# Performance work log

Hardware: AMD Instinct MI355X
Metric: run time of the kernel (lower is better)

Reference implementation:

```python
import jax, jax.numpy as jnp
import numpy as np

B, S, D, H = 8, 1024, 1024, 16
DK = D // H  # 64


def setup_inputs() -> dict:
    key = jax.random.key(0)
    ks = jax.random.split(key, 12)
    def w(k):
        return (jax.random.normal(k, (D, D), dtype=jnp.float32) * 0.02)
    def b(k):
        return (jax.random.normal(k, (D,), dtype=jnp.float32) * 0.02)
    return {
        "q": jax.random.normal(ks[0], (B, S, D), dtype=jnp.float32),
        "k": jax.random.normal(ks[1], (B, S, D), dtype=jnp.float32),
        "v": jax.random.normal(ks[2], (B, S, D), dtype=jnp.float32),
        "mask": jax.random.randint(ks[3], (B, 1, S, S), 0, 2, dtype=jnp.int32),
        "WQ_w": w(ks[4]), "WQ_b": b(ks[5]),
        "WK_w": w(ks[6]), "WK_b": b(ks[7]),
        "WV_w": w(ks[8]), "WV_b": b(ks[9]),
        "WO_w": w(ks[10]), "WO_b": b(ks[11]),
    }


def reference(q, k, v, mask, WQ_w, WQ_b, WK_w, WK_b, WV_w, WV_b, WO_w, WO_b):
    # nn.Linear: y = x @ W.T + b
    Q = (q @ WQ_w.T + WQ_b).reshape(B, S, H, DK)
    K = (k @ WK_w.T + WK_b).reshape(B, S, H, DK)
    V = (v @ WV_w.T + WV_b).reshape(B, S, H, DK)
    # scores: [B, H, Sq, Sk]
    scores = jnp.einsum("bqhd,bkhd->bhqk", Q, K) / jnp.sqrt(jnp.float32(DK))
    scores = jnp.where(mask == 0, jnp.float32(-1e9), scores)
    attn = jax.nn.softmax(scores, axis=-1)
    # dropout p=0.0 -> identity
    out = jnp.einsum("bhqk,bkhd->bqhd", attn, V).reshape(B, S, D)
    return out @ WO_w.T + WO_b
```

## Files before the change

### kernel.cpp

```cpp
#include <hip/hip_runtime.h>
#include <math.h>

typedef __bf16 bf16;
typedef __bf16 bf16x8 __attribute__((ext_vector_type(8)));
typedef __bf16 bf16x4 __attribute__((ext_vector_type(4)));
typedef float f32x4 __attribute__((ext_vector_type(4)));
typedef float f32x16 __attribute__((ext_vector_type(16)));
typedef int i32x4 __attribute__((ext_vector_type(4)));

constexpr int B_ = 8, S_ = 1024, D_ = 1024, H_ = 16, DK_ = 64;
constexpr int M_ = B_ * S_;
constexpr size_t A8 = (size_t)1 << 23;
constexpr size_t W1 = (size_t)1 << 20;
constexpr float QSCALE = 0.18033688011112042f;

#if __has_builtin(__builtin_amdgcn_exp2f)
#define EXP2F(x) __builtin_amdgcn_exp2f(x)
#else
#define EXP2F(x) exp2f(x)
#endif
#if __has_builtin(__builtin_amdgcn_rcpf)
#define RCPF(x) __builtin_amdgcn_rcpf(x)
#else
#define RCPF(x) (1.0f / (x))
#endif

#define GAS(p) ((const __attribute__((address_space(1))) void*)(p))
#define LAS(p) ((__attribute__((address_space(3))) void*)(p))

__device__ __forceinline__ float xor32f(float v, int bpidx) {
    return __builtin_bit_cast(float,
        __builtin_amdgcn_ds_bpermute(bpidx, __builtin_bit_cast(int, v)));
}
__device__ __forceinline__ int xor32i(int v, int bpidx) {
    return __builtin_amdgcn_ds_bpermute(bpidx, v);
}
__device__ __forceinline__ int pack_bf16(bf16 lo, bf16 hi) {
    return (int)(unsigned)__builtin_bit_cast(unsigned short, lo)
         | ((int)(unsigned)__builtin_bit_cast(unsigned short, hi) << 16);
}

struct F4Q { f32x4 a, b, c, d; };

__global__ __launch_bounds__(256) void cvt_all(
    const float* __restrict__ q, const float* __restrict__ k,
    const float* __restrict__ v, const float* __restrict__ w0,
    const float* __restrict__ w1, const float* __restrict__ w2,
    const float* __restrict__ w3, bf16* __restrict__ dst)
{
    size_t e = ((size_t)blockIdx.x * 256 + threadIdx.x) * 8;
    const float* src;
    size_t off;
    if (e < 3 * A8) {
        int t = (int)(e >> 23);
        src = (t == 0) ? q : (t == 1) ? k : v;
        off = e & (A8 - 1);
    } else {
        size_t ew = e - 3 * A8;
        int t = (int)(ew >> 20);
        src = (t == 0) ? w0 : (t == 1) ? w1 : (t == 2) ? w2 : w3;
        off = ew & (W1 - 1);
    }
    float4 a = *(const float4*)(src + off);
    float4 b = *(const float4*)(src + off + 4);
    bf16x8 o = { (bf16)a.x, (bf16)a.y, (bf16)a.z, (bf16)a.w,
                 (bf16)b.x, (bf16)b.y, (bf16)b.z, (bf16)b.w };
    *(bf16x8*)(dst + e) = o;
}

__global__ __launch_bounds__(256) void mask_cvt(
    const int* __restrict__ mask, float* __restrict__ mf)
{
    const int bx = blockIdx.x;
    const int kt = bx & 15, qt = (bx >> 4) & 7, b = bx >> 7;
    const int tid = threadIdx.x;
    const int w = tid >> 6, lane = tid & 63;
    const int hi = lane >> 5, l31 = lane & 31;
    const int q = qt * 128 + w * 32 + l31;

    const int* src = mask + ((size_t)b << 20) + (size_t)q * 1024 + kt * 64 + hi * 4;
    float* dst = mf + (size_t)bx * 8192 + w * 2048 + lane * 4;
#pragma unroll
    for (int blk = 0; blk < 2; ++blk)
#pragma unroll
        for (int rr = 0; rr < 4; ++rr) {
            int4 m = *(const int4*)(src + blk * 32 + rr * 8);
            f32x4 o = { m.x ? 0.f : -1e9f, m.y ? 0.f : -1e9f,
                        m.z ? 0.f : -1e9f, m.w ? 0.f : -1e9f };
            *(f32x4*)(dst + (blk * 4 + rr) * 256) = o;
        }
}

template<int OUT_MODE>
__global__ __launch_bounds__(256) void gemm_mfma(
    const bf16* __restrict__ X, const bf16* __restrict__ W,
    const float* __restrict__ bias, void* __restrict__ outv, float oscale)
{
    constexpr int K = 1024;
    __shared__ bf16 As[128 * 32];
    __shared__ bf16 Bs[128 * 32];

    const int tid  = threadIdx.x;
    const int lane = tid & 63;
    const int w    = tid >> 6;
    const int wm   = w & 1, wn = w >> 1;
    const int quad = lane >> 4, l15 = lane & 15;
    const int bm = blockIdx.x * 128, bn = blockIdx.y * 128;

    f32x4 acc[4][4];
#pragma unroll
    for (int i = 0; i < 4; ++i)
#pragma unroll
        for (int j = 0; j < 4; ++j)
#pragma unroll
            for (int r = 0; r < 4; ++r) acc[i][j][r] = 0.f;

    const int lrow = lane >> 2;
    const int lcol = (lane & 3) * 8;

    for (int k0 = 0; k0 < K; k0 += 32) {
        __syncthreads();
#pragma unroll
        for (int i = 0; i < 2; ++i) {
            const int rbase = w * 16 + i * 64;
            __builtin_amdgcn_global_load_lds(
                GAS(X + (size_t)(bm + rbase + lrow) * K + k0 + lcol),
                LAS(As + rbase * 32), 16, 0, 0);
            __builtin_amdgcn_global_load_lds(
                GAS(W + (size_t)(bn + rbase + lrow) * K + k0 + lcol),
                LAS(Bs + rbase * 32), 16, 0, 0);
        }
        __syncthreads();

        bf16x8 a[4], b[4];
#pragma unroll
        for (int i = 0; i < 4; ++i)
            a[i] = *(const bf16x8*)(As + (wm * 64 + i * 16 + l15) * 32 + quad * 8);
#pragma unroll
        for (int j = 0; j < 4; ++j)
            b[j] = *(const bf16x8*)(Bs + (wn * 64 + j * 16 + l15) * 32 + quad * 8);
#pragma unroll
        for (int i = 0; i < 4; ++i)
#pragma unroll
            for (int j = 0; j < 4; ++j)
                acc[i][j] = __builtin_amdgcn_mfma_f32_16x16x32_bf16(
                    a[i], b[j], acc[i][j], 0, 0, 0);
    }

#pragma unroll
    for (int i = 0; i < 4; ++i) {
#pragma unroll
        for (int j = 0; j < 4; ++j) {
            const int n = bn + wn * 64 + j * 16 + l15;
            const float bs = bias[n];
            if (OUT_MODE == 2) {
                const int m0 = bm + wm * 64 + i * 16 + quad * 4;
                const int bb = m0 >> 10, s0 = m0 & 1023;
                const int h = n >> 6, dk = n & 63;
                bf16x4 o;
#pragma unroll
                for (int r = 0; r < 4; ++r) o[r] = (bf16)(acc[i][j][r] + bs);
                *(bf16x4*)((bf16*)outv + (((size_t)(bb * 16 + h) * 64 + dk) << 10) + s0) = o;
            } else {
#pragma unroll
                for (int r = 0; r < 4; ++r) {
                    const int m = bm + wm * 64 + i * 16 + quad * 4 + r;
                    const float val = acc[i][j][r] + bs;
                    if (OUT_MODE == 0) {
                        ((float*)outv)[(size_t)m * 1024 + n] = val;
                    } else {
                        const int bb = m >> 10, s = m & 1023;
                        const int h = n >> 6, dk = n & 63;
                        ((bf16*)outv)[(((size_t)(bb * 16 + h)) * 1024 + s) * 64 + dk] =
                            (bf16)(val * oscale);
                    }
                }
            }
        }
    }
}

__global__ __launch_bounds__(256) void attn_mfma(
    const bf16* __restrict__ Q, const bf16* __restrict__ Kt,
    const bf16* __restrict__ Vt, const float* __restrict__ mf,
    bf16* __restrict__ out)
{
    __shared__ bf16 smem[2 * 2 * 4096];

    const int tid  = threadIdx.x;
    const int lane = tid & 63;
    const int w    = tid >> 6;
    const int hi   = lane >> 5, l31 = lane & 31;

    const int wid = (blockIdx.x & 7) * 128 + (blockIdx.x >> 3);
    const int qt = wid & 7;
    const int h  = (wid >> 3) & 15;
    const int b  = wid >> 7;

    const bf16* Qg  = Q + ((size_t)((b * H_ + h) * S_) + qt * 128 + w * 32) * DK_;
    const char* Kgh = (const char*)(Kt + (size_t)(b * H_ + h) * S_ * DK_);
    const char* Vgh = (const char*)(Vt + ((size_t)(b * H_ + h) << 16));
    const float* mtb = mf + (size_t)((b * 8 + qt) * 16) * 8192 + w * 2048 + lane * 4;

    const int tA = tid,        rA = tA >> 3, cA = (tA & 7) * 16;
    const int tB = 256 + tid,  rB = tB >> 3, cB = (tB & 7) * 16;
    const int kSrcA = rA * 128  + (cA ^ ((rA & 7) << 4));
    const int kSrcB = rB * 128  + (cB ^ ((rB & 7) << 4));
    const int vSrcA = rA * 2048 + (cA ^ ((rA & 7) << 4));
    const int vSrcB = rB * 2048 + (cB ^ ((rB & 7) << 4));

    auto stage = [&](int buf, int tkt) {
        bf16* Ks = smem + buf * 8192;
        bf16* Vs = Ks + 4096;
        const char* kg = Kgh + (size_t)tkt * 8192;
        const char* vg = Vgh + (size_t)tkt * 128;
        __builtin_amdgcn_global_load_lds(GAS(kg + kSrcA), LAS(Ks + w * 512),        16, 0, 0);
        __builtin_amdgcn_global_load_lds(GAS(kg + kSrcB), LAS(Ks + 2048 + w * 512), 16, 0, 0);
        __builtin_amdgcn_global_load_lds(GAS(vg + vSrcA), LAS(Vs + w * 512),        16, 0, 0);
        __builtin_amdgcn_global_load_lds(GAS(vg + vSrcB), LAS(Vs + 2048 + w * 512), 16, 0, 0);
    };

    stage(0, 0);

    bf16x8 qf[4];
#pragma unroll
    for (int ks = 0; ks < 4; ++ks)
        qf[ks] = *(const bf16x8*)(Qg + (size_t)l31 * 64 + ks * 16 + hi * 8);

    f32x4 mreg[8];
#pragma unroll
    for (int i = 0; i < 8; ++i) mreg[i] = *(const f32x4*)(mtb + i * 256);

    f32x16 O0, O1;
#pragma unroll
    for (int r = 0; r < 16; ++r) { O0[r] = 0.f; O1[r] = 0.f; }
    float mrow = -INFINITY, lrowv = 0.f;
    const int bpidx = (lane ^ 32) << 2;
    const int swz = (l31 & 7) << 4;

    __syncthreads();

#pragma unroll 2
    for (int kt = 0; kt < 16; ++kt) {
        const int buf = kt & 1;
        const bf16* Ks = smem + buf * 8192;
        const bf16* Vs = Ks + 4096;
        const char* KsB = (const char*)Ks;
        const char* VsB = (const char*)Vs;

        F4Q mq0 = { mreg[0], mreg[1], mreg[2], mreg[3] };
        F4Q mq1 = { mreg[4], mreg[5], mreg[6], mreg[7] };
        f32x16 acc0 = __builtin_bit_cast(f32x16, mq0);
        f32x16 acc1 = __builtin_bit_cast(f32x16, mq1);

        if (kt < 15) {
            const float* mkn = mtb + (size_t)(kt + 1) * 8192;
#pragma unroll
            for (int i = 0; i < 8; ++i) mreg[i] = *(const f32x4*)(mkn + i * 256);
        }

        if (kt + 1 < 16) stage(buf ^ 1, kt + 1);

#pragma unroll
        for (int ks = 0; ks < 4; ++ks) {
            const int cb = ks * 32 + hi * 16;
            bf16x8 k0 = *(const bf16x8*)(KsB + l31 * 128        + (cb ^ swz));
            bf16x8 k1 = *(const bf16x8*)(KsB + (l31 + 32) * 128 + (cb ^ swz));
            acc0 = __builtin_amdgcn_mfma_f32_32x32x16_bf16(k0, qf[ks], acc0, 0, 0, 0);
            acc1 = __builtin_amdgcn_mfma_f32_32x32x16_bf16(k1, qf[ks], acc1, 0, 0, 0);
        }

        float red[8];
#pragma unroll
        for (int i = 0; i < 8; ++i)
            red[i] = fmaxf(fmaxf(acc0[i], acc0[i + 8]), fmaxf(acc1[i], acc1[i + 8]));
#pragma unroll
        for (int i = 0; i < 4; ++i) red[i] = fmaxf(red[i], red[i + 4]);
        float mx = fmaxf(fmaxf(red[0], red[1]), fmaxf(red[2], red[3]));
        mx = fmaxf(mx, xor32f(mx, bpidx));

        if (__any(mx > mrow + 8.0f)) {
            const float mn = fmaxf(mrow, mx);
            const float alpha = EXP2F(mrow - mn);
            mrow = mn;
            lrowv *= alpha;
#pragma unroll
            for (int r = 0; r < 16; ++r) { O0[r] *= alpha; O1[r] *= alpha; }
        }

#pragma unroll
        for (int r = 0; r < 16; ++r) acc0[r] = EXP2F(acc0[r] - mrow);
#pragma unroll
        for (int r = 0; r < 16; ++r) acc1[r] = EXP2F(acc1[r] - mrow);

        int wd0[8], wd1[8];
        float ps = 0.f;
#pragma unroll
        for (int s = 0; s < 8; ++s) {
            bf16 e0 = (bf16)acc0[2 * s], o0 = (bf16)acc0[2 * s + 1];
            bf16 e1 = (bf16)acc1[2 * s], o1 = (bf16)acc1[2 * s + 1];
            ps += (float)e0 + (float)o0 + (float)e1 + (float)o1;
            wd0[s] = pack_bf16(e0, o0);
            wd1[s] = pack_bf16(e1, o1);
        }
        ps += xor32f(ps, bpidx);
        lrowv += ps;

#pragma unroll
        for (int ks = 0; ks < 4; ++ks) {
            const int s0 = (ks & 1) * 4;
            int p0, p1, p2, p3;
            if (ks < 2) { p0 = wd0[s0]; p1 = wd0[s0 + 1]; p2 = wd0[s0 + 2]; p3 = wd0[s0 + 3]; }
            else        { p0 = wd1[s0]; p1 = wd1[s0 + 1]; p2 = wd1[s0 + 2]; p3 = wd1[s0 + 3]; }
            const int rx = xor32i(hi ? p0 : p2, bpidx);
            const int ry = xor32i(hi ? p1 : p3, bpidx);
            i32x4 pw = { hi ? rx : p0, hi ? ry : p1, hi ? p2 : rx, hi ? p3 : ry };
            bf16x8 pa = __builtin_bit_cast(bf16x8, pw);

            const int cb = ks * 32 + hi * 16;
            bf16x8 v0 = *(const bf16x8*)(VsB + l31 * 128        + (cb ^ swz));
            bf16x8 v1 = *(const bf16x8*)(VsB + (l31 + 32) * 128 + (cb ^ swz));
            O0 = __builtin_amdgcn_mfma_f32_32x32x16_bf16(v0, pa, O0, 0, 0, 0);
            O1 = __builtin_amdgcn_mfma_f32_32x32x16_bf16(v1, pa, O1, 0, 0, 0);
        }
        __syncthreads();
    }

    const float rinv = RCPF(lrowv);
    bf16* og = out + ((size_t)b * S_ + qt * 128 + w * 32 + l31) * D_ + h * DK_;
#pragma unroll
    for (int rr = 0; rr < 4; ++rr) {
        bf16x4 o0 = { (bf16)(O0[rr * 4 + 0] * rinv), (bf16)(O0[rr * 4 + 1] * rinv),
                      (bf16)(O0[rr * 4 + 2] * rinv), (bf16)(O0[rr * 4 + 3] * rinv) };
        bf16x4 o1 = { (bf16)(O1[rr * 4 + 0] * rinv), (bf16)(O1[rr * 4 + 1] * rinv),
                      (bf16)(O1[rr * 4 + 2] * rinv), (bf16)(O1[rr * 4 + 3] * rinv) };
        *(bf16x4*)(og + rr * 8 + hi * 4)      = o0;
        *(bf16x4*)(og + 32 + rr * 8 + hi * 4) = o1;
    }
}

extern "C" void kernel_launch(void* const* d_in, const int* in_sizes, int n_in,
                              void* d_out, int out_size, void* d_ws, size_t ws_size,
                              hipStream_t stream) {
    const float* q    = (const float*)d_in[0];
    const float* k    = (const float*)d_in[1];
    const float* v    = (const float*)d_in[2];
    const int*   mask = (const int*)d_in[3];
    const float* WQw  = (const float*)d_in[4];
    const float* WQb  = (const float*)d_in[5];
    const float* WKw  = (const float*)d_in[6];
    const float* WKb  = (const float*)d_in[7];
    const float* WVw  = (const float*)d_in[8];
    const float* WVb  = (const float*)d_in[9];
    const float* WOw  = (const float*)d_in[10];
    const float* WOb  = (const float*)d_in[11];

    bf16* ws = (bf16*)d_ws;
    bf16* qb  = ws;
    bf16* kb  = qb + A8;
    bf16* vb  = kb + A8;
    bf16* wqb = vb + A8;
    bf16* wkb = wqb + W1;
    bf16* wvb = wkb + W1;
    bf16* wob = wvb + W1;
    bf16* Qp  = wob + W1;
    bf16* Kp  = Qp + A8;
    bf16* Vp  = Kp + A8;
    float* maskf = (float*)qb;
    bf16* AO     = vb;

    cvt_all<<<dim3(14336), 256, 0, stream>>>(q, k, v, WQw, WKw, WVw, WOw, ws);

    dim3 gg(M_ / 128, D_ / 128);
    gemm_mfma<1><<<gg, 256, 0, stream>>>(qb, wqb, WQb, (void*)Qp, QSCALE);
    gemm_mfma<1><<<gg, 256, 0, stream>>>(kb, wkb, WKb, (void*)Kp, 1.0f);
    gemm_mfma<2><<<gg, 256, 0, stream>>>(vb, wvb, WVb, (void*)Vp, 1.0f);

    mask_cvt<<<dim3(1024), 256, 0, stream>>>(mask, maskf);

    attn_mfma<<<dim3(1024), 256, 0, stream>>>(Qp, Kp, Vp, maskf, AO);

    gemm_mfma<0><<<gg, 256, 0, stream>>>(AO, wob, WOb, d_out, 1.0f);
}
```

Measured before the change: 363.7 us.

## Merge QKV projections into one launch and tune attention inner loop

Folds the three separate Q/K/V projection GEMM launches into a single 1536-block launch that picks its operands by block index, and gives the output projection its own non-templated kernel. The attention kernel gets launch_bounds occupancy 4, s_setprio raised around the MFMA sections, a vectorised elementwise-max reduction, and a row sum taken from the packed bf16 words instead of converting each value back to float. These target launch overhead and tail effects in the projections and VALU cost in the softmax. The occupancy hint may force register spills, and the setprio and reduction changes could just as easily slow things down.

```diff
diff --git a/kernel.cpp b/kernel.cpp
--- a/kernel.cpp
+++ b/kernel.cpp
@@ -4,8 +4,11 @@
 typedef __bf16 bf16;
 typedef __bf16 bf16x8 __attribute__((ext_vector_type(8)));
 typedef __bf16 bf16x4 __attribute__((ext_vector_type(4)));
+typedef float f32x2 __attribute__((ext_vector_type(2)));
 typedef float f32x4 __attribute__((ext_vector_type(4)));
+typedef float f32x8 __attribute__((ext_vector_type(8)));
 typedef float f32x16 __attribute__((ext_vector_type(16)));
+typedef int i32x2 __attribute__((ext_vector_type(2)));
 typedef int i32x4 __attribute__((ext_vector_type(4)));
 
 constexpr int B_ = 8, S_ = 1024, D_ = 1024, H_ = 16, DK_ = 64;
@@ -91,21 +94,33 @@
         }
 }
 
-template<int OUT_MODE>
-__global__ __launch_bounds__(256) void gemm_mfma(
-    const bf16* __restrict__ X, const bf16* __restrict__ W,
-    const float* __restrict__ bias, void* __restrict__ outv, float oscale)
+__global__ __launch_bounds__(256) void qkv_gemm(
+    const bf16* __restrict__ qb, const bf16* __restrict__ kb,
+    const bf16* __restrict__ vb, const bf16* __restrict__ wq,
+    const bf16* __restrict__ wk, const bf16* __restrict__ wv,
+    const float* __restrict__ bq, const float* __restrict__ bk,
+    const float* __restrict__ bv, bf16* __restrict__ Qp,
+    bf16* __restrict__ Kp, bf16* __restrict__ Vp, float qscale)
 {
     constexpr int K = 1024;
     __shared__ bf16 As[128 * 32];
     __shared__ bf16 Bs[128 * 32];
+
+    const int bid = blockIdx.x;
+    const int which = bid >> 9;
+    const int gb = bid & 511;
+    const bf16* X = which == 0 ? qb : which == 1 ? kb : vb;
+    const bf16* W = which == 0 ? wq : which == 1 ? wk : wv;
+    const float* bias = which == 0 ? bq : which == 1 ? bk : bv;
+    bf16* outp = which == 0 ? Qp : which == 1 ? Kp : Vp;
+    const float oscale = which == 0 ? qscale : 1.0f;
 
     const int tid  = threadIdx.x;
     const int lane = tid & 63;
     const int w    = tid >> 6;
     const int wm   = w & 1, wn = w >> 1;
     const int quad = lane >> 4, l15 = lane & 15;
-    const int bm = blockIdx.x * 128, bn = blockIdx.y * 128;
+    const int bm = (gb & 63) * 128, bn = (gb >> 6) * 128;
 
     f32x4 acc[4][4];
 #pragma unroll
@@ -153,34 +168,98 @@
         for (int j = 0; j < 4; ++j) {
             const int n = bn + wn * 64 + j * 16 + l15;
             const float bs = bias[n];
-            if (OUT_MODE == 2) {
+            if (which == 2) {
                 const int m0 = bm + wm * 64 + i * 16 + quad * 4;
                 const int bb = m0 >> 10, s0 = m0 & 1023;
                 const int h = n >> 6, dk = n & 63;
                 bf16x4 o;
 #pragma unroll
                 for (int r = 0; r < 4; ++r) o[r] = (bf16)(acc[i][j][r] + bs);
-                *(bf16x4*)((bf16*)outv + (((size_t)(bb * 16 + h) * 64 + dk) << 10) + s0) = o;
+                *(bf16x4*)(outp + (((size_t)(bb * 16 + h) * 64 + dk) << 10) + s0) = o;
             } else {
 #pragma unroll
                 for (int r = 0; r < 4; ++r) {
                     const int m = bm + wm * 64 + i * 16 + quad * 4 + r;
-                    const float val = acc[i][j][r] + bs;
-                    if (OUT_MODE == 0) {
-                        ((float*)outv)[(size_t)m * 1024 + n] = val;
-                    } else {
-                        const int bb = m >> 10, s = m & 1023;
-                        const int h = n >> 6, dk = n & 63;
-                        ((bf16*)outv)[(((size_t)(bb * 16 + h)) * 1024 + s) * 64 + dk] =
-                            (bf16)(val * oscale);
-                    }
+                    const int bb = m >> 10, s = m & 1023;
+                    const int h = n >> 6, dk = n & 63;
+                    outp[(((size_t)(bb * 16 + h)) * 1024 + s) * 64 + dk] =
+                        (bf16)((acc[i][j][r] + bs) * oscale);
                 }
             }
         }
     }
 }
 
-__global__ __launch_bounds__(256) void attn_mfma(
+__global__ __launch_bounds__(256) void gemm_out(
+    const bf16* __restrict__ X, const bf16* __restrict__ W,
+    const float* __restrict__ bias, float* __restrict__ outv)
+{
+    constexpr int K = 1024;
+    __shared__ bf16 As[128 * 32];
+    __shared__ bf16 Bs[128 * 32];
+
+    const int tid  = threadIdx.x;
+    const int lane = tid & 63;
+    const int w    = tid >> 6;
+    const int wm   = w & 1, wn = w >> 1;
+    const int quad = lane >> 4, l15 = lane & 15;
+    const int bm = blockIdx.x * 128, bn = blockIdx.y * 128;
+
+    f32x4 acc[4][4];
+#pragma unroll
+    for (int i = 0; i < 4; ++i)
+#pragma unroll
+        for (int j = 0; j < 4; ++j)
+#pragma unroll
+            for (int r = 0; r < 4; ++r) acc[i][j][r] = 0.f;
+
+    const int lrow = lane >> 2;
+    const int lcol = (lane & 3) * 8;
+
+    for (int k0 = 0; k0 < K; k0 += 32) {
+        __syncthreads();
+#pragma unroll
+        for (int i = 0; i < 2; ++i) {
+            const int rbase = w * 16 + i * 64;
+            __builtin_amdgcn_global_load_lds(
+                GAS(X + (size_t)(bm + rbase + lrow) * K + k0 + lcol),
+                LAS(As + rbase * 32), 16, 0, 0);
+            __builtin_amdgcn_global_load_lds(
+                GAS(W + (size_t)(bn + rbase + lrow) * K + k0 + lcol),
+                LAS(Bs + rbase * 32), 16, 0, 0);
+        }
+        __syncthreads();
+
+        bf16x8 a[4], b[4];
+#pragma unroll
+        for (int i = 0; i < 4; ++i)
+            a[i] = *(const bf16x8*)(As + (wm * 64 + i * 16 + l15) * 32 + quad * 8);
+#pragma unroll
+        for (int j = 0; j < 4; ++j)
+            b[j] = *(const bf16x8*)(Bs + (wn * 64 + j * 16 + l15) * 32 + quad * 8);
+#pragma unroll
+        for (int i = 0; i < 4; ++i)
+#pragma unroll
+            for (int j = 0; j < 4; ++j)
+                acc[i][j] = __builtin_amdgcn_mfma_f32_16x16x32_bf16(
+                    a[i], b[j], acc[i][j], 0, 0, 0);
+    }
+
+#pragma unroll
+    for (int i = 0; i < 4; ++i)
+#pragma unroll
+        for (int j = 0; j < 4; ++j) {
+            const int n = bn + wn * 64 + j * 16 + l15;
+            const float bs = bias[n];
+#pragma unroll
+            for (int r = 0; r < 4; ++r) {
+                const int m = bm + wm * 64 + i * 16 + quad * 4 + r;
+                outv[(size_t)m * 1024 + n] = acc[i][j][r] + bs;
+            }
+        }
+}
+
+__global__ __launch_bounds__(256, 4) void attn_mfma(
     const bf16* __restrict__ Q, const bf16* __restrict__ Kt,
     const bf16* __restrict__ Vt, const float* __restrict__ mf,
     bf16* __restrict__ out)
@@ -261,6 +340,7 @@
 
         if (kt + 1 < 16) stage(buf ^ 1, kt + 1);
 
+        __builtin_amdgcn_s_setprio(1);
 #pragma unroll
         for (int ks = 0; ks < 4; ++ks) {
             const int cb = ks * 32 + hi * 16;
@@ -269,7 +349,21 @@
             acc0 = __builtin_amdgcn_mfma_f32_32x32x16_bf16(k0, qf[ks], acc0, 0, 0, 0);
             acc1 = __builtin_amdgcn_mfma_f32_32x32x16_bf16(k1, qf[ks], acc1, 0, 0, 0);
         }
-
+        __builtin_amdgcn_s_setprio(0);
+
+#if __has_builtin(__builtin_elementwise_max)
+        f32x16 m16 = __builtin_elementwise_max(acc0, acc1);
+        f32x8 m8 = __builtin_elementwise_max(
+            __builtin_shufflevector(m16, m16, 0, 1, 2, 3, 4, 5, 6, 7),
+            __builtin_shufflevector(m16, m16, 8, 9, 10, 11, 12, 13, 14, 15));
+        f32x4 m4 = __builtin_elementwise_max(
+            __builtin_shufflevector(m8, m8, 0, 1, 2, 3),
+            __builtin_shufflevector(m8, m8, 4, 5, 6, 7));
+        f32x2 m2 = __builtin_elementwise_max(
+            __builtin_shufflevector(m4, m4, 0, 1),
+            __builtin_shufflevector(m4, m4, 2, 3));
+        float mx = fmaxf(m2[0], m2[1]);
+#else
         float red[8];
 #pragma unroll
         for (int i = 0; i < 8; ++i)
@@ -277,6 +371,7 @@
 #pragma unroll
         for (int i = 0; i < 4; ++i) red[i] = fmaxf(red[i], red[i + 4]);
         float mx = fmaxf(fmaxf(red[0], red[1]), fmaxf(red[2], red[3]));
+#endif
         mx = fmaxf(mx, xor32f(mx, bpidx));
 
         if (__any(mx > mrow + 8.0f)) {
@@ -284,28 +379,36 @@
             const float alpha = EXP2F(mrow - mn);
             mrow = mn;
             lrowv *= alpha;
-#pragma unroll
-            for (int r = 0; r < 16; ++r) { O0[r] *= alpha; O1[r] *= alpha; }
-        }
-
-#pragma unroll
-        for (int r = 0; r < 16; ++r) acc0[r] = EXP2F(acc0[r] - mrow);
-#pragma unroll
-        for (int r = 0; r < 16; ++r) acc1[r] = EXP2F(acc1[r] - mrow);
+            O0 *= alpha;
+            O1 *= alpha;
+        }
+
+        acc0 -= mrow;
+        acc1 -= mrow;
+#pragma unroll
+        for (int r = 0; r < 16; ++r) acc0[r] = EXP2F(acc0[r]);
+#pragma unroll
+        for (int r = 0; r < 16; ++r) acc1[r] = EXP2F(acc1[r]);
 
         int wd0[8], wd1[8];
-        float ps = 0.f;
 #pragma unroll
         for (int s = 0; s < 8; ++s) {
-            bf16 e0 = (bf16)acc0[2 * s], o0 = (bf16)acc0[2 * s + 1];
-            bf16 e1 = (bf16)acc1[2 * s], o1 = (bf16)acc1[2 * s + 1];
-            ps += (float)e0 + (float)o0 + (float)e1 + (float)o1;
-            wd0[s] = pack_bf16(e0, o0);
-            wd1[s] = pack_bf16(e1, o1);
-        }
+            wd0[s] = pack_bf16((bf16)acc0[2 * s], (bf16)acc0[2 * s + 1]);
+            wd1[s] = pack_bf16((bf16)acc1[2 * s], (bf16)acc1[2 * s + 1]);
+        }
+        f32x2 ps2 = { 0.f, 0.f };
+#pragma unroll
+        for (int s = 0; s < 8; ++s) {
+            i32x2 t0 = { wd0[s] << 16, (int)(wd0[s] & 0xffff0000) };
+            i32x2 t1 = { wd1[s] << 16, (int)(wd1[s] & 0xffff0000) };
+            ps2 += __builtin_bit_cast(f32x2, t0);
+            ps2 += __builtin_bit_cast(f32x2, t1);
+        }
+        float ps = ps2[0] + ps2[1];
         ps += xor32f(ps, bpidx);
         lrowv += ps;
 
+        __builtin_amdgcn_s_setprio(1);
 #pragma unroll
         for (int ks = 0; ks < 4; ++ks) {
             const int s0 = (ks & 1) * 4;
@@ -323,6 +426,7 @@
             O0 = __builtin_amdgcn_mfma_f32_32x32x16_bf16(v0, pa, O0, 0, 0, 0);
             O1 = __builtin_amdgcn_mfma_f32_32x32x16_bf16(v1, pa, O1, 0, 0, 0);
         }
+        __builtin_amdgcn_s_setprio(0);
         __syncthreads();
     }
 
@@ -371,14 +475,12 @@
 
     cvt_all<<<dim3(14336), 256, 0, stream>>>(q, k, v, WQw, WKw, WVw, WOw, ws);
 
-    dim3 gg(M_ / 128, D_ / 128);
-    gemm_mfma<1><<<gg, 256, 0, stream>>>(qb, wqb, WQb, (void*)Qp, QSCALE);
-    gemm_mfma<1><<<gg, 256, 0, stream>>>(kb, wkb, WKb, (void*)Kp, 1.0f);
-    gemm_mfma<2><<<gg, 256, 0, stream>>>(vb, wvb, WVb, (void*)Vp, 1.0f);
+    qkv_gemm<<<dim3(1536), 256, 0, stream>>>(qb, kb, vb, wqb, wkb, wvb,
+                                             WQb, WKb, WVb, Qp, Kp, Vp, QSCALE);
 
     mask_cvt<<<dim3(1024), 256, 0, stream>>>(mask, maskf);
 
     attn_mfma<<<dim3(1024), 256, 0, stream>>>(Qp, Kp, Vp, maskf, AO);
 
-    gemm_mfma<0><<<gg, 256, 0, stream>>>(AO, wob, WOb, d_out, 1.0f);
-}
+    gemm_out<<<dim3(M_ / 128, D_ / 128), 256, 0, stream>>>(AO, wob, WOb, (float*)d_out);
+}
```

New measurement: 398.5 us. 9.6% more time.
